# Performance work log

Measured on AMD Instinct MI355X. Metric: run time of the kernel, lower is better.

## Reference

```python
import jax, jax.numpy as jnp
import numpy as np

B, P, N, H = 2, 512, 8, 32
INIT_RANGE = 0.02


def setup_inputs() -> dict:
    key = jax.random.key(0)
    k1, k2, k3 = jax.random.split(key, 3)
    d = jax.random.normal(k1, (B, P, N, H), dtype=jnp.float32)
    e = jax.random.normal(k2, (B, P, N, H), dtype=jnp.float32)
    W = jax.random.normal(k3, (N, H, H, H), dtype=jnp.float32) * INIT_RANGE
    return {"d": d, "e": e, "W": W}


def reference(d, e, W):
    # Trilinear contraction: v[b,p1,p2,n,h3] = sum_{h1,h2} d[b,p1,n,h1] e[b,p2,n,h2] W[n,h1,h2,h3]
    # Decompose into two batched matmuls to avoid the naive 4-way product:
    # tmp[b,p1,n,h2,h3] = sum_h1 d[b,p1,n,h1] W[n,h1,h2,h3]
    tmp = jnp.einsum('bpni,nijk->bpnjk', d, W)
    # v[b,p1,p2,n,h3] = sum_h2 tmp[b,p1,n,h2,h3] e[b,p2,n,h2]
    v = jnp.einsum('bpnjk,bqnj->bpqnk', tmp, e)
    return v
```

## Files before the change

kernel.cpp:

```cpp
#include <hip/hip_runtime.h>

#define BB 2
#define PP 512
#define NN 8
#define HH 32

typedef float f4     __attribute__((ext_vector_type(4)));
typedef float f32x4  __attribute__((ext_vector_type(4)));
typedef short bf16x8 __attribute__((ext_vector_type(8)));

__device__ __forceinline__ short f2bf(float f) {
  union { float f; unsigned u; } v; v.f = f;
  unsigned r = v.u + 0x7FFFu + ((v.u >> 16) & 1u);
  return (short)(r >> 16);
}

__global__ __launch_bounds__(256) void wtrans_kernel(
    const float* __restrict__ W, float* __restrict__ WT) {
  const int blk = blockIdx.x;
  const int t   = threadIdx.x;
  __shared__ float ls[32][33];
  const float* src = W  + (size_t)blk * 1024;
  float*       dst = WT + (size_t)blk * 1024;
  #pragma unroll
  for (int r = 0; r < 4; ++r) {
    const int h2 = r * 8 + (t >> 5), h3 = t & 31;
    ls[h2][h3] = src[h2 * 32 + h3];
  }
  __syncthreads();
  #pragma unroll
  for (int r = 0; r < 4; ++r) {
    const int h3 = r * 8 + (t >> 5), h2 = t & 31;
    dst[h3 * 32 + h2] = ls[h2][h3];
  }
}

__global__ __launch_bounds__(256) void prep2_kernel(
    const float* __restrict__ d, const float* __restrict__ WT,
    short* __restrict__ tmpT) {
  const int bid    = blockIdx.x;
  const int b      = bid >> 8;
  const int rem    = bid & 255;
  const int npair  = rem >> 6;
  const int p1base = (rem & 63) * 8;
  const int t      = threadIdx.x;

  __shared__ float dsh[2][32][8];
  {
    const int h1 = t & 31, p1l = (t >> 5) & 7;
    #pragma unroll
    for (int r = 0; r < 2; ++r)
      dsh[r][h1][p1l] =
          d[(size_t)((b * PP + p1base + p1l) * NN + npair * 2 + r) * HH + h1];
  }
  __syncthreads();

  const int np  = t >> 7;
  const int h3  = (t >> 2) & 31;
  const int h2g = t & 3;
  const int n   = npair * 2 + np;

  float acc[8][8];
  #pragma unroll
  for (int p = 0; p < 8; ++p)
    #pragma unroll
    for (int q = 0; q < 8; ++q) acc[p][q] = 0.f;

  const float* wb = WT + ((size_t)(n * HH) * HH + h3) * HH + h2g * 8;
  for (int h1 = 0; h1 < 32; ++h1) {
    const f4 w0 = *(const f4*)(wb + (size_t)h1 * 1024);
    const f4 w1 = *(const f4*)(wb + (size_t)h1 * 1024 + 4);
    const f4 d0 = *(const f4*)&dsh[np][h1][0];
    const f4 d1 = *(const f4*)&dsh[np][h1][4];
    #pragma unroll
    for (int p = 0; p < 4; ++p) {
      #pragma unroll
      for (int q = 0; q < 4; ++q) {
        acc[p][q]         = fmaf(d0[p], w0[q], acc[p][q]);
        acc[p][q + 4]     = fmaf(d0[p], w1[q], acc[p][q + 4]);
        acc[p + 4][q]     = fmaf(d1[p], w0[q], acc[p + 4][q]);
        acc[p + 4][q + 4] = fmaf(d1[p], w1[q], acc[p + 4][q + 4]);
      }
    }
  }

  const size_t obase =
      ((size_t)(b * PP + p1base) * NN + n) * (HH * HH) + h3 * 32 + h2g * 8;
  #pragma unroll
  for (int p = 0; p < 8; ++p) {
    bf16x8 v;
    #pragma unroll
    for (int q = 0; q < 8; ++q) v[q] = f2bf(acc[p][q]);
    *(bf16x8*)(tmpT + obase + (size_t)p * (NN * HH * HH)) = v;
  }
}

__global__ __launch_bounds__(256) void ecvt_kernel(
    const float* __restrict__ e, short* __restrict__ eB) {
  const int i = (blockIdx.x * 256 + threadIdx.x) * 8;
  const f4 e0 = *(const f4*)(e + i);
  const f4 e1 = *(const f4*)(e + i + 4);
  bf16x8 v;
  v[0] = f2bf(e0[0]); v[1] = f2bf(e0[1]); v[2] = f2bf(e0[2]); v[3] = f2bf(e0[3]);
  v[4] = f2bf(e1[0]); v[5] = f2bf(e1[1]); v[6] = f2bf(e1[2]); v[7] = f2bf(e1[3]);
  *(bf16x8*)(eB + i) = v;
}

__global__ __launch_bounds__(256, 4) void vmain_kernel(
    const short* __restrict__ eB, const short* __restrict__ tmpT,
    float* __restrict__ out) {
  const int bid = blockIdx.x;
  const int b   = bid >> 9;
  const int p1  = bid & 511;
  const int t   = threadIdx.x;
  const int wv  = t >> 6;
  const int l   = t & 63;
  const int lr  = l & 15;
  const int lk  = l >> 4;

  __shared__ float lbuf[4][16][128];
  float* wl = &lbuf[wv][0][0];

  bf16x8 bfr[8][2];
  const short* tb = tmpT + (size_t)(b * PP + p1) * (NN * HH * HH);
  #pragma unroll
  for (int n = 0; n < 8; ++n)
    #pragma unroll
    for (int c = 0; c < 2; ++c)
      bfr[n][c] = *(const bf16x8*)(tb + n * (HH * HH) + (c * 16 + lr) * 32 + lk * 8);

  const short* ebb  = eB + (size_t)b * (PP * NN * HH);
  float*       outb = out + (size_t)(b * PP + p1) * (PP * NN * HH);
  const f32x4  z    = {0.f, 0.f, 0.f, 0.f};

  for (int i = 0; i < 8; ++i) {
    const int m0 = (wv * 8 + i) * 16;
    #pragma unroll
    for (int half = 0; half < 2; ++half) {
      const int n0 = half * 4;
      #pragma unroll
      for (int nn = 0; nn < 4; ++nn) {
        const int n = n0 + nn;
        const bf16x8 a =
            *(const bf16x8*)(ebb + (size_t)((m0 + lr) * NN + n) * HH + lk * 8);
        const f32x4 c0 = __builtin_amdgcn_mfma_f32_16x16x32_bf16(bfr[n][0], a, z, 0, 0, 0);
        const f32x4 c1 = __builtin_amdgcn_mfma_f32_16x16x32_bf16(bfr[n][1], a, z, 0, 0, 0);
        const int s0 = (nn * 8 + lk)     ^ (lr & 7);
        const int s1 = (nn * 8 + 4 + lk) ^ (lr & 7);
        *(f32x4*)(wl + lr * 128 + s0 * 4) = c0;
        *(f32x4*)(wl + lr * 128 + s1 * 4) = c1;
      }
      #pragma unroll
      for (int j = 0; j < 8; ++j) {
        const int row  = 2 * j + (l >> 5);
        const int slot = l & 31;
        const f32x4 v = *(const f32x4*)(wl + row * 128 + ((slot ^ (row & 7)) * 4));
        *(f32x4*)(outb + (size_t)(m0 + row) * (NN * HH) + n0 * HH + slot * 4) = v;
      }
    }
  }
}

__global__ __launch_bounds__(256, 4) void fused_kernel(
    const float* __restrict__ d, const float* __restrict__ e,
    const float* __restrict__ W, float* __restrict__ out) {
  const int bid = blockIdx.x;
  const int b   = bid >> 9;
  const int p1  = bid & 511;
  const int t   = threadIdx.x;

  __shared__ float dsh[NN * HH];
  __shared__ short tsh[NN * HH * HH];
  dsh[t] = d[(size_t)(b * PP + p1) * (NN * HH) + t];
  __syncthreads();

  const int h3  = t & 31;
  const int h2b = t >> 5;
  for (int n = 0; n < 8; ++n) {
    f4 dv[8];
    #pragma unroll
    for (int j = 0; j < 8; ++j) dv[j] = *(const f4*)&dsh[n * 32 + j * 4];
    const float* Wn = W + (size_t)n * (HH * HH * HH);
    #pragma unroll
    for (int h2s = 0; h2s < 4; ++h2s) {
      const int h2 = h2s * 8 + h2b;
      float acc = 0.f;
      #pragma unroll
      for (int j = 0; j < 8; ++j)
        #pragma unroll
        for (int k = 0; k < 4; ++k)
          acc = fmaf(dv[j][k], Wn[(j * 4 + k) * 1024 + h2 * 32 + h3], acc);
      tsh[n * 1024 + h3 * 32 + h2] = f2bf(acc);
    }
  }
  __syncthreads();

  const int wv = t >> 6;
  const int l  = t & 63;
  const int lr = l & 15;
  const int lk = l >> 4;
  bf16x8 bfr[8][2];
  #pragma unroll
  for (int n = 0; n < 8; ++n)
    #pragma unroll
    for (int c = 0; c < 2; ++c)
      bfr[n][c] = *(const bf16x8*)&tsh[n * (HH * HH) + (c * 16 + lr) * 32 + lk * 8];

  const float* eb   = e + (size_t)b * (PP * NN * HH);
  float*       outb = out + (size_t)(b * PP + p1) * (PP * NN * HH);
  const f32x4  z    = {0.f, 0.f, 0.f, 0.f};
  for (int i = 0; i < 8; ++i) {
    const int m0 = (wv * 8 + i) * 16;
    #pragma unroll
    for (int n = 0; n < 8; ++n) {
      const float* ep = eb + (size_t)(((m0 + lr) * NN + n) * HH + lk * 8);
      const f4 e0 = *(const f4*)ep;
      const f4 e1 = *(const f4*)(ep + 4);
      bf16x8 a;
      a[0] = f2bf(e0[0]); a[1] = f2bf(e0[1]); a[2] = f2bf(e0[2]); a[3] = f2bf(e0[3]);
      a[4] = f2bf(e1[0]); a[5] = f2bf(e1[1]); a[6] = f2bf(e1[2]); a[7] = f2bf(e1[3]);
      const f32x4 c0 = __builtin_amdgcn_mfma_f32_16x16x32_bf16(bfr[n][0], a, z, 0, 0, 0);
      const f32x4 c1 = __builtin_amdgcn_mfma_f32_16x16x32_bf16(bfr[n][1], a, z, 0, 0, 0);
      float* op = outb + (size_t)(m0 + lr) * (NN * HH) + n * HH + lk * 4;
      *(f32x4*)op        = c0;
      *(f32x4*)(op + 16) = c1;
    }
  }
}

extern "C" void kernel_launch(void* const* d_in, const int* in_sizes, int n_in,
                              void* d_out, int out_size, void* d_ws, size_t ws_size,
                              hipStream_t stream) {
  const float* d = (const float*)d_in[0];
  const float* e = (const float*)d_in[1];
  const float* W = (const float*)d_in[2];
  float* out = (float*)d_out;

  const size_t tmp_bytes = (size_t)BB * PP * NN * HH * HH * sizeof(short);
  const size_t eb_bytes  = (size_t)BB * PP * NN * HH * sizeof(short);
  const size_t wt_bytes  = (size_t)NN * HH * HH * HH * sizeof(float);
  if (ws_size >= tmp_bytes + eb_bytes + wt_bytes) {
    short* tmpT = (short*)d_ws;
    short* eB   = (short*)((char*)d_ws + tmp_bytes);
    float* WT   = (float*)((char*)d_ws + tmp_bytes + eb_bytes);
    wtrans_kernel<<<dim3(NN * HH), dim3(256), 0, stream>>>(W, WT);
    ecvt_kernel<<<dim3(BB * PP * NN * HH / (256 * 8)), dim3(256), 0, stream>>>(e, eB);
    prep2_kernel<<<dim3(BB * 4 * (PP / 8)), dim3(256), 0, stream>>>(d, WT, tmpT);
    vmain_kernel<<<dim3(BB * PP), dim3(256), 0, stream>>>(eB, tmpT, out);
  } else {
    fused_kernel<<<dim3(BB * PP), dim3(256), 0, stream>>>(d, e, W, out);
  }
}
```

Measured before the change: 131.2 us.

## Fuse tmp computation into main kernel and merge W-transpose with e-convert

The d×W contraction moves out of a separate prep kernel that wrote a bf16 tmp tensor to global memory and into the main kernel. Each block now computes its own 8×32×32 tmp slice into shared memory, reusing the output staging buffer. The W transpose and the e-to-bf16 conversion are merged into one auxiliary launch, so there are two launches instead of four. This removes the 16 MB tmp round trip and two launch overheads. In exchange each block redoes a 256K-FMA scalar contraction that reads WT from global memory, which lengthens its prologue.

```diff
diff --git a/kernel.cpp b/kernel.cpp
--- a/kernel.cpp
+++ b/kernel.cpp
@@ -15,100 +15,41 @@
   return (short)(r >> 16);
 }
 
-__global__ __launch_bounds__(256) void wtrans_kernel(
-    const float* __restrict__ W, float* __restrict__ WT) {
-  const int blk = blockIdx.x;
+__global__ __launch_bounds__(256) void aux_kernel(
+    const float* __restrict__ W, const float* __restrict__ e,
+    float* __restrict__ WT, short* __restrict__ eB) {
+  const int bid = blockIdx.x;
   const int t   = threadIdx.x;
-  __shared__ float ls[32][33];
-  const float* src = W  + (size_t)blk * 1024;
-  float*       dst = WT + (size_t)blk * 1024;
-  #pragma unroll
-  for (int r = 0; r < 4; ++r) {
-    const int h2 = r * 8 + (t >> 5), h3 = t & 31;
-    ls[h2][h3] = src[h2 * 32 + h3];
-  }
-  __syncthreads();
-  #pragma unroll
-  for (int r = 0; r < 4; ++r) {
-    const int h3 = r * 8 + (t >> 5), h2 = t & 31;
-    dst[h3 * 32 + h2] = ls[h2][h3];
-  }
-}
-
-__global__ __launch_bounds__(256) void prep2_kernel(
+
+  if (bid < 256) {
+    __shared__ float ls[32][33];
+    const float* src = W  + (size_t)bid * 1024;
+    float*       dst = WT + (size_t)bid * 1024;
+    #pragma unroll
+    for (int r = 0; r < 4; ++r) {
+      const int h2 = r * 8 + (t >> 5), h3 = t & 31;
+      ls[h2][h3] = src[h2 * 32 + h3];
+    }
+    __syncthreads();
+    #pragma unroll
+    for (int r = 0; r < 4; ++r) {
+      const int h3 = r * 8 + (t >> 5), h2 = t & 31;
+      dst[h3 * 32 + h2] = ls[h2][h3];
+    }
+  } else {
+    const int i = ((bid - 256) * 256 + t) * 8;
+    const f4 e0 = *(const f4*)(e + i);
+    const f4 e1 = *(const f4*)(e + i + 4);
+    bf16x8 v;
+    v[0] = f2bf(e0[0]); v[1] = f2bf(e0[1]); v[2] = f2bf(e0[2]); v[3] = f2bf(e0[3]);
+    v[4] = f2bf(e1[0]); v[5] = f2bf(e1[1]); v[6] = f2bf(e1[2]); v[7] = f2bf(e1[3]);
+    *(bf16x8*)(eB + i) = v;
+  }
+}
+
+__global__ __launch_bounds__(256, 4) void vmain_kernel(
     const float* __restrict__ d, const float* __restrict__ WT,
-    short* __restrict__ tmpT) {
-  const int bid    = blockIdx.x;
-  const int b      = bid >> 8;
-  const int rem    = bid & 255;
-  const int npair  = rem >> 6;
-  const int p1base = (rem & 63) * 8;
-  const int t      = threadIdx.x;
-
-  __shared__ float dsh[2][32][8];
-  {
-    const int h1 = t & 31, p1l = (t >> 5) & 7;
-    #pragma unroll
-    for (int r = 0; r < 2; ++r)
-      dsh[r][h1][p1l] =
-          d[(size_t)((b * PP + p1base + p1l) * NN + npair * 2 + r) * HH + h1];
-  }
-  __syncthreads();
-
-  const int np  = t >> 7;
-  const int h3  = (t >> 2) & 31;
-  const int h2g = t & 3;
-  const int n   = npair * 2 + np;
-
-  float acc[8][8];
-  #pragma unroll
-  for (int p = 0; p < 8; ++p)
-    #pragma unroll
-    for (int q = 0; q < 8; ++q) acc[p][q] = 0.f;
-
-  const float* wb = WT + ((size_t)(n * HH) * HH + h3) * HH + h2g * 8;
-  for (int h1 = 0; h1 < 32; ++h1) {
-    const f4 w0 = *(const f4*)(wb + (size_t)h1 * 1024);
-    const f4 w1 = *(const f4*)(wb + (size_t)h1 * 1024 + 4);
-    const f4 d0 = *(const f4*)&dsh[np][h1][0];
-    const f4 d1 = *(const f4*)&dsh[np][h1][4];
-    #pragma unroll
-    for (int p = 0; p < 4; ++p) {
-      #pragma unroll
-      for (int q = 0; q < 4; ++q) {
-        acc[p][q]         = fmaf(d0[p], w0[q], acc[p][q]);
-        acc[p][q + 4]     = fmaf(d0[p], w1[q], acc[p][q + 4]);
-        acc[p + 4][q]     = fmaf(d1[p], w0[q], acc[p + 4][q]);
-        acc[p + 4][q + 4] = fmaf(d1[p], w1[q], acc[p + 4][q + 4]);
-      }
-    }
-  }
-
-  const size_t obase =
-      ((size_t)(b * PP + p1base) * NN + n) * (HH * HH) + h3 * 32 + h2g * 8;
-  #pragma unroll
-  for (int p = 0; p < 8; ++p) {
-    bf16x8 v;
-    #pragma unroll
-    for (int q = 0; q < 8; ++q) v[q] = f2bf(acc[p][q]);
-    *(bf16x8*)(tmpT + obase + (size_t)p * (NN * HH * HH)) = v;
-  }
-}
-
-__global__ __launch_bounds__(256) void ecvt_kernel(
-    const float* __restrict__ e, short* __restrict__ eB) {
-  const int i = (blockIdx.x * 256 + threadIdx.x) * 8;
-  const f4 e0 = *(const f4*)(e + i);
-  const f4 e1 = *(const f4*)(e + i + 4);
-  bf16x8 v;
-  v[0] = f2bf(e0[0]); v[1] = f2bf(e0[1]); v[2] = f2bf(e0[2]); v[3] = f2bf(e0[3]);
-  v[4] = f2bf(e1[0]); v[5] = f2bf(e1[1]); v[6] = f2bf(e1[2]); v[7] = f2bf(e1[3]);
-  *(bf16x8*)(eB + i) = v;
-}
-
-__global__ __launch_bounds__(256, 4) void vmain_kernel(
-    const short* __restrict__ eB, const short* __restrict__ tmpT,
-    float* __restrict__ out) {
+    const short* __restrict__ eB, float* __restrict__ out) {
   const int bid = blockIdx.x;
   const int b   = bid >> 9;
   const int p1  = bid & 511;
@@ -119,16 +60,49 @@
   const int lk  = l >> 4;
 
   __shared__ float lbuf[4][16][128];
-  float* wl = &lbuf[wv][0][0];
+  __shared__ float dsh[NN * HH];
+  short* tsh = (short*)&lbuf[0][0][0];
+
+  dsh[t] = d[(size_t)(b * PP + p1) * (NN * HH) + t];
+  __syncthreads();
+
+  {
+    const int n_p = t >> 5, h3_p = t & 31;
+    float acc[32];
+    #pragma unroll
+    for (int q = 0; q < 32; ++q) acc[q] = 0.f;
+    const float* wtb = WT + (size_t)n_p * 32768 + h3_p * 32;
+    for (int h1 = 0; h1 < 32; ++h1) {
+      const float dval = dsh[n_p * 32 + h1];
+      const float* wrow = wtb + (size_t)h1 * 1024;
+      #pragma unroll
+      for (int g = 0; g < 8; ++g) {
+        const f4 w = *(const f4*)(wrow + g * 4);
+        acc[g * 4 + 0] = fmaf(dval, w[0], acc[g * 4 + 0]);
+        acc[g * 4 + 1] = fmaf(dval, w[1], acc[g * 4 + 1]);
+        acc[g * 4 + 2] = fmaf(dval, w[2], acc[g * 4 + 2]);
+        acc[g * 4 + 3] = fmaf(dval, w[3], acc[g * 4 + 3]);
+      }
+    }
+    #pragma unroll
+    for (int g = 0; g < 4; ++g) {
+      bf16x8 v;
+      #pragma unroll
+      for (int q = 0; q < 8; ++q) v[q] = f2bf(acc[g * 8 + q]);
+      *(bf16x8*)(tsh + n_p * 1024 + h3_p * 32 + g * 8) = v;
+    }
+  }
+  __syncthreads();
 
   bf16x8 bfr[8][2];
-  const short* tb = tmpT + (size_t)(b * PP + p1) * (NN * HH * HH);
   #pragma unroll
   for (int n = 0; n < 8; ++n)
     #pragma unroll
     for (int c = 0; c < 2; ++c)
-      bfr[n][c] = *(const bf16x8*)(tb + n * (HH * HH) + (c * 16 + lr) * 32 + lk * 8);
-
+      bfr[n][c] = *(const bf16x8*)(tsh + n * 1024 + (c * 16 + lr) * 32 + lk * 8);
+  __syncthreads();
+
+  float* wl = &lbuf[wv][0][0];
   const short* ebb  = eB + (size_t)b * (PP * NN * HH);
   float*       outb = out + (size_t)(b * PP + p1) * (PP * NN * HH);
   const f32x4  z    = {0.f, 0.f, 0.f, 0.f};
@@ -236,17 +210,13 @@
   const float* W = (const float*)d_in[2];
   float* out = (float*)d_out;
 
-  const size_t tmp_bytes = (size_t)BB * PP * NN * HH * HH * sizeof(short);
-  const size_t eb_bytes  = (size_t)BB * PP * NN * HH * sizeof(short);
-  const size_t wt_bytes  = (size_t)NN * HH * HH * HH * sizeof(float);
-  if (ws_size >= tmp_bytes + eb_bytes + wt_bytes) {
-    short* tmpT = (short*)d_ws;
-    short* eB   = (short*)((char*)d_ws + tmp_bytes);
-    float* WT   = (float*)((char*)d_ws + tmp_bytes + eb_bytes);
-    wtrans_kernel<<<dim3(NN * HH), dim3(256), 0, stream>>>(W, WT);
-    ecvt_kernel<<<dim3(BB * PP * NN * HH / (256 * 8)), dim3(256), 0, stream>>>(e, eB);
-    prep2_kernel<<<dim3(BB * 4 * (PP / 8)), dim3(256), 0, stream>>>(d, WT, tmpT);
-    vmain_kernel<<<dim3(BB * PP), dim3(256), 0, stream>>>(eB, tmpT, out);
+  const size_t wt_bytes = (size_t)NN * HH * HH * HH * sizeof(float);
+  const size_t eb_bytes = (size_t)BB * PP * NN * HH * sizeof(short);
+  if (ws_size >= wt_bytes + eb_bytes) {
+    float* WT = (float*)d_ws;
+    short* eB = (short*)((char*)d_ws + wt_bytes);
+    aux_kernel<<<dim3(256 + 128), dim3(256), 0, stream>>>(W, e, WT, eB);
+    vmain_kernel<<<dim3(BB * PP), dim3(256), 0, stream>>>(d, WT, eB, out);
   } else {
     fused_kernel<<<dim3(BB * PP), dim3(256), 0, stream>>>(d, e, W, out);
   }
```

Result: slower. 334.1 us (+154.6%).

## Merge W-transpose and e-convert kernels, pre-swizzle e into MFMA layout, cut vmain registers

Applied to the files above, without the earlier changes.

Folds the W transpose and the bf16 conversion of e into a single aux kernel, removing one launch. e is stored in a fragment-ordered layout so each lane in vmain reads one contiguous 16-byte chunk. vmain no longer keeps all 16 tmp fragments in registers; it reloads them per pair of heads, halves the LDS staging buffer and raises launch bounds to 8 blocks per CU for higher occupancy. The cost is repeated global/L2 reads of the tmp fragments inside the loop.

```diff
diff --git a/kernel.cpp b/kernel.cpp
--- a/kernel.cpp
+++ b/kernel.cpp
@@ -15,23 +15,41 @@
   return (short)(r >> 16);
 }
 
-__global__ __launch_bounds__(256) void wtrans_kernel(
-    const float* __restrict__ W, float* __restrict__ WT) {
-  const int blk = blockIdx.x;
+__global__ __launch_bounds__(256) void aux_kernel(
+    const float* __restrict__ W, const float* __restrict__ e,
+    float* __restrict__ WT, short* __restrict__ eBf) {
+  const int bid = blockIdx.x;
   const int t   = threadIdx.x;
-  __shared__ float ls[32][33];
-  const float* src = W  + (size_t)blk * 1024;
-  float*       dst = WT + (size_t)blk * 1024;
-  #pragma unroll
-  for (int r = 0; r < 4; ++r) {
-    const int h2 = r * 8 + (t >> 5), h3 = t & 31;
-    ls[h2][h3] = src[h2 * 32 + h3];
-  }
-  __syncthreads();
-  #pragma unroll
-  for (int r = 0; r < 4; ++r) {
-    const int h3 = r * 8 + (t >> 5), h2 = t & 31;
-    dst[h3 * 32 + h2] = ls[h2][h3];
+
+  if (bid < 256) {
+    __shared__ float ls[32][33];
+    const float* src = W  + (size_t)bid * 1024;
+    float*       dst = WT + (size_t)bid * 1024;
+    #pragma unroll
+    for (int r = 0; r < 4; ++r) {
+      const int h2 = r * 8 + (t >> 5), h3 = t & 31;
+      ls[h2][h3] = src[h2 * 32 + h3];
+    }
+    __syncthreads();
+    #pragma unroll
+    for (int r = 0; r < 4; ++r) {
+      const int h3 = r * 8 + (t >> 5), h2 = t & 31;
+      dst[h3 * 32 + h2] = ls[h2][h3];
+    }
+  } else {
+    const int ft = (bid - 256) * 256 + t;
+    const int l  = ft & 63;
+    const int n  = (ft >> 6) & 7;
+    const int pt = (ft >> 9) & 31;
+    const int b  = ft >> 14;
+    const float* src =
+        e + (((size_t)(b * PP + pt * 16 + (l & 15)) * NN + n) * HH + (l >> 4) * 8);
+    const f4 e0 = *(const f4*)src;
+    const f4 e1 = *(const f4*)(src + 4);
+    bf16x8 v;
+    v[0] = f2bf(e0[0]); v[1] = f2bf(e0[1]); v[2] = f2bf(e0[2]); v[3] = f2bf(e0[3]);
+    v[4] = f2bf(e1[0]); v[5] = f2bf(e1[1]); v[6] = f2bf(e1[2]); v[7] = f2bf(e1[3]);
+    *(bf16x8*)(eBf + (size_t)ft * 8) = v;
   }
 }
 
@@ -95,19 +113,8 @@
   }
 }
 
-__global__ __launch_bounds__(256) void ecvt_kernel(
-    const float* __restrict__ e, short* __restrict__ eB) {
-  const int i = (blockIdx.x * 256 + threadIdx.x) * 8;
-  const f4 e0 = *(const f4*)(e + i);
-  const f4 e1 = *(const f4*)(e + i + 4);
-  bf16x8 v;
-  v[0] = f2bf(e0[0]); v[1] = f2bf(e0[1]); v[2] = f2bf(e0[2]); v[3] = f2bf(e0[3]);
-  v[4] = f2bf(e1[0]); v[5] = f2bf(e1[1]); v[6] = f2bf(e1[2]); v[7] = f2bf(e1[3]);
-  *(bf16x8*)(eB + i) = v;
-}
-
-__global__ __launch_bounds__(256, 4) void vmain_kernel(
-    const short* __restrict__ eB, const short* __restrict__ tmpT,
+__global__ __launch_bounds__(256, 8) void vmain_kernel(
+    const short* __restrict__ eBf, const short* __restrict__ tmpT,
     float* __restrict__ out) {
   const int bid = blockIdx.x;
   const int b   = bid >> 9;
@@ -118,44 +125,39 @@
   const int lr  = l & 15;
   const int lk  = l >> 4;
 
-  __shared__ float lbuf[4][16][128];
-  float* wl = &lbuf[wv][0][0];
-
-  bf16x8 bfr[8][2];
-  const short* tb = tmpT + (size_t)(b * PP + p1) * (NN * HH * HH);
-  #pragma unroll
-  for (int n = 0; n < 8; ++n)
-    #pragma unroll
-    for (int c = 0; c < 2; ++c)
-      bfr[n][c] = *(const bf16x8*)(tb + n * (HH * HH) + (c * 16 + lr) * 32 + lk * 8);
-
-  const short* ebb  = eB + (size_t)b * (PP * NN * HH);
+  __shared__ float lbuf[4][16][64];
+  float*       wl   = &lbuf[wv][0][0];
+  const short* tb   = tmpT + (size_t)(b * PP + p1) * (NN * HH * HH);
+  const short* eb   = eBf + (size_t)b * (32 * NN * 512);
   float*       outb = out + (size_t)(b * PP + p1) * (PP * NN * HH);
   const f32x4  z    = {0.f, 0.f, 0.f, 0.f};
+  const int    sw   = lr & 7;
 
   for (int i = 0; i < 8; ++i) {
-    const int m0 = (wv * 8 + i) * 16;
-    #pragma unroll
-    for (int half = 0; half < 2; ++half) {
-      const int n0 = half * 4;
+    const int pt = wv * 8 + i;
+    const int m0 = pt * 16;
+    #pragma unroll
+    for (int q = 0; q < 4; ++q) {
+      const int n0 = q * 2;
+      const bf16x8 f00 = *(const bf16x8*)(tb + (n0 + 0) * 1024 + lr * 32 + lk * 8);
+      const bf16x8 f01 = *(const bf16x8*)(tb + (n0 + 0) * 1024 + (16 + lr) * 32 + lk * 8);
+      const bf16x8 f10 = *(const bf16x8*)(tb + (n0 + 1) * 1024 + lr * 32 + lk * 8);
+      const bf16x8 f11 = *(const bf16x8*)(tb + (n0 + 1) * 1024 + (16 + lr) * 32 + lk * 8);
+      const bf16x8 a0 = *(const bf16x8*)(eb + ((size_t)(pt * NN + n0) << 9) + l * 8);
+      const bf16x8 a1 = *(const bf16x8*)(eb + ((size_t)(pt * NN + n0 + 1) << 9) + l * 8);
+      const f32x4 c00 = __builtin_amdgcn_mfma_f32_16x16x32_bf16(f00, a0, z, 0, 0, 0);
+      const f32x4 c01 = __builtin_amdgcn_mfma_f32_16x16x32_bf16(f01, a0, z, 0, 0, 0);
+      const f32x4 c10 = __builtin_amdgcn_mfma_f32_16x16x32_bf16(f10, a1, z, 0, 0, 0);
+      const f32x4 c11 = __builtin_amdgcn_mfma_f32_16x16x32_bf16(f11, a1, z, 0, 0, 0);
+      *(f32x4*)(wl + lr * 64 + ((lk)      ^ sw) * 4) = c00;
+      *(f32x4*)(wl + lr * 64 + ((4 + lk)  ^ sw) * 4) = c01;
+      *(f32x4*)(wl + lr * 64 + ((8 + lk)  ^ sw) * 4) = c10;
+      *(f32x4*)(wl + lr * 64 + ((12 + lk) ^ sw) * 4) = c11;
       #pragma unroll
-      for (int nn = 0; nn < 4; ++nn) {
-        const int n = n0 + nn;
-        const bf16x8 a =
-            *(const bf16x8*)(ebb + (size_t)((m0 + lr) * NN + n) * HH + lk * 8);
-        const f32x4 c0 = __builtin_amdgcn_mfma_f32_16x16x32_bf16(bfr[n][0], a, z, 0, 0, 0);
-        const f32x4 c1 = __builtin_amdgcn_mfma_f32_16x16x32_bf16(bfr[n][1], a, z, 0, 0, 0);
-        const int s0 = (nn * 8 + lk)     ^ (lr & 7);
-        const int s1 = (nn * 8 + 4 + lk) ^ (lr & 7);
-        *(f32x4*)(wl + lr * 128 + s0 * 4) = c0;
-        *(f32x4*)(wl + lr * 128 + s1 * 4) = c1;
-      }
-      #pragma unroll
-      for (int j = 0; j < 8; ++j) {
-        const int row  = 2 * j + (l >> 5);
-        const int slot = l & 31;
-        const f32x4 v = *(const f32x4*)(wl + row * 128 + ((slot ^ (row & 7)) * 4));
-        *(f32x4*)(outb + (size_t)(m0 + row) * (NN * HH) + n0 * HH + slot * 4) = v;
+      for (int j = 0; j < 4; ++j) {
+        const int row = 4 * j + lk;
+        const f32x4 v = *(const f32x4*)(wl + row * 64 + ((lr ^ (row & 7)) * 4));
+        *(f32x4*)(outb + (size_t)(m0 + row) * (NN * HH) + n0 * HH + lr * 4) = v;
       }
     }
   }
@@ -241,12 +243,11 @@
   const size_t wt_bytes  = (size_t)NN * HH * HH * HH * sizeof(float);
   if (ws_size >= tmp_bytes + eb_bytes + wt_bytes) {
     short* tmpT = (short*)d_ws;
-    short* eB   = (short*)((char*)d_ws + tmp_bytes);
+    short* eBf  = (short*)((char*)d_ws + tmp_bytes);
     float* WT   = (float*)((char*)d_ws + tmp_bytes + eb_bytes);
-    wtrans_kernel<<<dim3(NN * HH), dim3(256), 0, stream>>>(W, WT);
-    ecvt_kernel<<<dim3(BB * PP * NN * HH / (256 * 8)), dim3(256), 0, stream>>>(e, eB);
-    prep2_kernel<<<dim3(BB * 4 * (PP / 8)), dim3(256), 0, stream>>>(d, WT, tmpT);
-    vmain_kernel<<<dim3(BB * PP), dim3(256), 0, stream>>>(eB, tmpT, out);
+    aux_kernel<<<dim3(256 + 128), dim3(256), 0, stream>>>(W, e, WT, eBf);
+    prep2_kernel<<<dim3(512), dim3(256), 0, stream>>>(d, WT, tmpT);
+    vmain_kernel<<<dim3(BB * PP), dim3(256), 0, stream>>>(eBf, tmpT, out);
   } else {
     fused_kernel<<<dim3(BB * PP), dim3(256), 0, stream>>>(d, e, W, out);
   }
```

New measurement: 165.6 us. 26.2% more time.
